# Kernel tuning notes

Measured on AMD Instinct MI355X. Metric: run time of the kernel, lower is better.

The kernel has to match this reference:

```python
import jax, jax.numpy as jnp
import numpy as np

EMB_DIM = 1024
N_HEADS = 16
HEAD_DIM = EMB_DIM // N_HEADS


def setup_inputs() -> dict:
    key = jax.random.key(0)
    ks = jax.random.split(key, 6)
    B, S, D = 2, 2048, EMB_DIM
    scale = 1.0 / np.sqrt(D)
    return {
        "in_data": jax.random.normal(ks[0], (B, S, D), dtype=jnp.float32),
        "Wq": jax.random.normal(ks[1], (D, D), dtype=jnp.float32) * scale,
        "Wk": jax.random.normal(ks[2], (D, D), dtype=jnp.float32) * scale,
        "Wv": jax.random.normal(ks[3], (D, D), dtype=jnp.float32) * scale,
        "Wo": jax.random.normal(ks[4], (D, D), dtype=jnp.float32) * scale,
        "bo": jax.random.normal(ks[5], (D,), dtype=jnp.float32) * 0.01,
    }


def reference(in_data, Wq, Wk, Wv, Wo, bo):
    B, S, D = in_data.shape
    H, Hd = N_HEADS, HEAD_DIM
    # Linear projections (qvbias=False): torch Linear is x @ W.T
    q = in_data @ Wq.T
    k = in_data @ Wk.T
    v = in_data @ Wv.T
    # split heads -> (B, H, S, Hd)
    q = q.reshape(B, S, H, Hd).transpose(0, 2, 1, 3)
    k = k.reshape(B, S, H, Hd).transpose(0, 2, 1, 3)
    v = v.reshape(B, S, H, Hd).transpose(0, 2, 1, 3)
    # scores (B, H, S, S), causal mask applied BEFORE scaling (as in source)
    scores = jnp.einsum("bhqd,bhkd->bhqk", q, k)
    causal = jnp.triu(jnp.ones((S, S), dtype=bool), k=1)
    scores = jnp.where(causal, -jnp.inf, scores)
    scores = scores / jnp.sqrt(jnp.asarray(Hd, dtype=scores.dtype))
    attn = jax.nn.softmax(scores, axis=-1)
    # dropout with drop_rate=0.0 -> identity
    ctx = jnp.einsum("bhqk,bhkd->bhqd", attn, v)
    ctx = ctx.transpose(0, 2, 1, 3).reshape(B, S, D)
    out = ctx @ Wo.T + bo
    return out
```

## Files before the change

kernel.cpp:

```cpp
#include <hip/hip_runtime.h>

typedef _Float16 f16;
typedef _Float16 f16x2 __attribute__((ext_vector_type(2)));
typedef _Float16 f16x4 __attribute__((ext_vector_type(4)));
typedef _Float16 f16x8 __attribute__((ext_vector_type(8)));
typedef float f32x4 __attribute__((ext_vector_type(4)));
typedef int i32x4 __attribute__((ext_vector_type(4)));

#define MFMA(a, b, c) __builtin_amdgcn_mfma_f32_16x16x32_f16((a), (b), (c), 0, 0, 0)

typedef __attribute__((address_space(1))) const void gvoid;
typedef __attribute__((address_space(3))) void lvoid;

__device__ __forceinline__ void gload16(const void* g, void* l) {
    __builtin_amdgcn_global_load_lds((gvoid*)g, (lvoid*)l, 16, 0, 0);
}

__global__ void cast_all(const float* __restrict__ x,
                         const float* __restrict__ w0, const float* __restrict__ w1,
                         const float* __restrict__ w2, const float* __restrict__ w3,
                         f16* __restrict__ xb, f16* __restrict__ wb) {
    const int NX = 4096 * 1024;
    int i = (blockIdx.x * 256 + threadIdx.x) * 4;
    if (i < NX) {
        float4 v = *(const float4*)(x + i);
        f16x4 o = {(f16)v.x, (f16)v.y, (f16)v.z, (f16)v.w};
        *(f16x4*)(xb + i) = o;
    } else {
        int j = i - NX;
        const float* s = (j < (1 << 20)) ? w0 : (j < (2 << 20)) ? w1
                       : (j < (3 << 20)) ? w2 : w3;
        int loc = j & ((1 << 20) - 1);
        float4 v = *(const float4*)(s + loc);
        f16x4 o = {(f16)v.x, (f16)v.y, (f16)v.z, (f16)v.w};
        *(f16x4*)(wb + j) = o;
    }
}

template <bool FINAL>
__global__ void gemm_bt(const f16* __restrict__ A, const f16* __restrict__ Bw,
                        f16* __restrict__ Cf, f16* __restrict__ VTo,
                        float* __restrict__ Co, const float* __restrict__ bias) {
    __shared__ __align__(16) f16 As[128 * 64];
    __shared__ __align__(16) f16 Bs[128 * 64];
    const int tid = threadIdx.x;
    const int lane = tid & 63, wid = tid >> 6;
    const int lo = lane & 15, hi = lane >> 4;
    const int wr = wid >> 1, wc = wid & 1;
    const int m0 = blockIdx.x * 128, n0 = blockIdx.y * 128;
    const char* Ab = (const char*)A;
    const char* Bb = (const char*)(Bw + (size_t)blockIdx.z * (1024 * 1024));

    f32x4 acc[4][4];
#pragma unroll
    for (int i = 0; i < 4; ++i)
#pragma unroll
        for (int j = 0; j < 4; ++j) acc[i][j] = (f32x4){0.f, 0.f, 0.f, 0.f};

    for (int kt = 0; kt < 16; ++kt) {
        const int kb = kt * 128;
#pragma unroll
        for (int rr = 0; rr < 4; ++rr) {
            int o = rr * 4096 + tid * 16;
            int row = o >> 7, colB = o & 127;
            gload16(Ab + (size_t)(m0 + row) * 2048 + kb + colB, (char*)As + o);
            gload16(Bb + (size_t)(n0 + row) * 2048 + kb + colB, (char*)Bs + o);
        }
        __syncthreads();
#pragma unroll
        for (int kc = 0; kc < 2; ++kc) {
            f16x8 af[4], bf[4];
#pragma unroll
            for (int f = 0; f < 4; ++f)
                af[f] = *(const f16x8*)(As + (wr * 64 + f * 16 + lo) * 64 + kc * 32 + hi * 8);
#pragma unroll
            for (int f = 0; f < 4; ++f)
                bf[f] = *(const f16x8*)(Bs + (wc * 64 + f * 16 + lo) * 64 + kc * 32 + hi * 8);
#pragma unroll
            for (int i = 0; i < 4; ++i)
#pragma unroll
                for (int j = 0; j < 4; ++j) acc[i][j] = MFMA(af[i], bf[j], acc[i][j]);
        }
        __syncthreads();
    }

    const int mbase = m0 + wr * 64 + hi * 4;
    const int nbase = n0 + wc * 64 + lo;
    if (FINAL) {
#pragma unroll
        for (int j = 0; j < 4; ++j) {
            float bj = bias[nbase + j * 16];
#pragma unroll
            for (int i = 0; i < 4; ++i)
#pragma unroll
                for (int r = 0; r < 4; ++r)
                    Co[(size_t)(mbase + i * 16 + r) * 1024 + nbase + j * 16] =
                        acc[i][j][r] + bj;
        }
    } else if (blockIdx.z == 2) {
#pragma unroll
        for (int i = 0; i < 4; ++i)
#pragma unroll
            for (int j = 0; j < 4; ++j)
#pragma unroll
                for (int r = 0; r < 4; ++r) {
                    int m = mbase + i * 16 + r, n = nbase + j * 16;
                    VTo[(size_t)((m >> 11) * 1024 + n) * 2048 + (m & 2047)] =
                        (f16)acc[i][j][r];
                }
    } else {
        const float osc = (blockIdx.z == 0) ? 0.18033688f : 1.0f;
        f16* Cz = Cf + (size_t)blockIdx.z * (4096 * 1024);
#pragma unroll
        for (int i = 0; i < 4; ++i)
#pragma unroll
            for (int j = 0; j < 4; ++j)
#pragma unroll
                for (int r = 0; r < 4; ++r)
                    Cz[(size_t)(mbase + i * 16 + r) * 1024 + nbase + j * 16] =
                        (f16)(acc[i][j][r] * osc);
    }
}

__global__ __launch_bounds__(256) void attn(const f16* __restrict__ Q,
                                            const f16* __restrict__ K,
                                            const f16* __restrict__ VT,
                                            f16* __restrict__ CTX) {
    __shared__ __align__(16) f16 K0[64 * 64];
    __shared__ __align__(16) f16 K1[64 * 64];
    __shared__ __align__(16) f16 V0[64 * 64];
    __shared__ __align__(16) f16 V1[64 * 64];
    const int tid = threadIdx.x;
    const int lane = tid & 63, w = tid >> 6;
    const int lo = lane & 15, hi = lane >> 4;
    const int bh = blockIdx.x;
    const int qt = 31 - blockIdx.y;
    const int b = bh >> 4, h = bh & 15;
    const int qw0 = qt * 64 + w * 16;
    const int qglob = qw0 + lo;

    const f16* qrow = Q + (size_t)(b * 2048 + qw0 + lo) * 1024 + h * 64 + hi * 8;
    const f16x8 qa0 = *(const f16x8*)(qrow);
    const f16x8 qa1 = *(const f16x8*)(qrow + 32);

    f32x4 ctx[4];
#pragma unroll
    for (int d = 0; d < 4; ++d) ctx[d] = (f32x4){0.f, 0.f, 0.f, 0.f};
    float mrun = -3e38f, lsum = 0.f;

    const int idx0 = (2 * (hi & 1)) * 16 + lo;
    const int idx1 = idx0 + 16;

    const char* Kb = (const char*)K;
    const char* Vb = (const char*)VT;

    auto stage = [&](f16* Kd, f16* Vd, int t) {
        const int kv0 = t * 64;
#pragma unroll
        for (int rr = 0; rr < 2; ++rr) {
            int o = rr * 4096 + tid * 16;
            int row = o >> 7;
            int colB = (o & 127) ^ ((row & 7) << 4);
            gload16(Kb + (size_t)(b * 2048 + kv0 + row) * 2048 + h * 128 + colB,
                    (char*)Kd + o);
            gload16(Vb + (size_t)(b * 1024 + h * 64 + row) * 4096 + (size_t)kv0 * 2 + colB,
                    (char*)Vd + o);
        }
    };

    auto compute = [&](const f16* Klb, const f16* Vlb, int t) {
        f32x4 s4[4];
        __builtin_amdgcn_s_setprio(1);
#pragma unroll
        for (int fj = 0; fj < 4; ++fj) {
            f32x4 a = (f32x4){0.f, 0.f, 0.f, 0.f};
            const int kv = fj * 16 + lo;
#pragma unroll
            for (int kc = 0; kc < 2; ++kc) {
                const int cb = (kc * 64 + hi * 16) ^ ((kv & 7) << 4);
                f16x8 kf = *(const f16x8*)((const char*)Klb + kv * 128 + cb);
                a = MFMA(kf, kc ? qa1 : qa0, a);
            }
            s4[fj] = a;
        }
        __builtin_amdgcn_s_setprio(0);

        float pv[16];
        if (t == qt) {
#pragma unroll
            for (int fj = 0; fj < 4; ++fj)
#pragma unroll
                for (int r = 0; r < 4; ++r) {
                    const int kvg = t * 64 + fj * 16 + hi * 4 + r;
                    pv[fj * 4 + r] = (kvg > qglob) ? -1e38f : s4[fj][r];
                }
        } else {
#pragma unroll
            for (int fj = 0; fj < 4; ++fj)
#pragma unroll
                for (int r = 0; r < 4; ++r) pv[fj * 4 + r] = s4[fj][r];
        }

        float tm[8];
#pragma unroll
        for (int i = 0; i < 8; ++i) tm[i] = fmaxf(pv[i], pv[i + 8]);
#pragma unroll
        for (int i = 0; i < 4; ++i) tm[i] = fmaxf(tm[i], tm[i + 4]);
        const float mxl = fmaxf(fmaxf(tm[0], tm[1]), fmaxf(tm[2], tm[3]));

        if (__any(mxl > mrun + 8.0f)) {
            float mxg = fmaxf(mxl, __shfl_xor(mxl, 16));
            mxg = fmaxf(mxg, __shfl_xor(mxg, 32));
            const float mnew = fmaxf(mrun, mxg);
            const float corr = __builtin_amdgcn_exp2f(mrun - mnew);
            mrun = mnew;
            lsum *= corr;
#pragma unroll
            for (int d = 0; d < 4; ++d) {
                ctx[d][0] *= corr; ctx[d][1] *= corr;
                ctx[d][2] *= corr; ctx[d][3] *= corr;
            }
        }

#pragma unroll
        for (int i = 0; i < 16; ++i) pv[i] = __builtin_amdgcn_exp2f(pv[i] - mrun);
        float ts[8];
#pragma unroll
        for (int i = 0; i < 8; ++i) ts[i] = pv[i] + pv[i + 8];
#pragma unroll
        for (int i = 0; i < 4; ++i) ts[i] = ts[i] + ts[i + 4];
        lsum += (ts[0] + ts[1]) + (ts[2] + ts[3]);

        int ph[4][2];
#pragma unroll
        for (int fj = 0; fj < 4; ++fj)
#pragma unroll
            for (int r2 = 0; r2 < 2; ++r2) {
                f16x2 hpair = {(f16)pv[fj * 4 + 2 * r2], (f16)pv[fj * 4 + 2 * r2 + 1]};
                ph[fj][r2] = __builtin_bit_cast(int, hpair);
            }

        f16x8 pb[2];
#pragma unroll
        for (int kc = 0; kc < 2; ++kc) {
            i32x4 dw;
#pragma unroll
            for (int j2 = 0; j2 < 4; ++j2) {
                const int idx = (j2 < 2) ? idx0 : idx1;
                int vA = __shfl(ph[2 * kc][j2 & 1], idx);
                int vB = __shfl(ph[2 * kc + 1][j2 & 1], idx);
                dw[j2] = (hi & 2) ? vB : vA;
            }
            pb[kc] = __builtin_bit_cast(f16x8, dw);
        }

        __builtin_amdgcn_s_setprio(1);
#pragma unroll
        for (int df = 0; df < 4; ++df) {
            const int d = df * 16 + lo;
#pragma unroll
            for (int kc = 0; kc < 2; ++kc) {
                const int cb = (kc * 64 + hi * 16) ^ ((d & 7) << 4);
                f16x8 vf = *(const f16x8*)((const char*)Vlb + d * 128 + cb);
                ctx[df] = MFMA(vf, pb[kc], ctx[df]);
            }
        }
        __builtin_amdgcn_s_setprio(0);
    };

    stage(&K0[0], &V0[0], 0);
    for (int t = 0; t <= qt; ++t) {
        __syncthreads();
        if ((t & 1) == 0) {
            if (t < qt) stage(&K1[0], &V1[0], t + 1);
            compute(&K0[0], &V0[0], t);
        } else {
            if (t < qt) stage(&K0[0], &V0[0], t + 1);
            compute(&K1[0], &V1[0], t);
        }
    }

    float lt = lsum + __shfl_xor(lsum, 16);
    lt += __shfl_xor(lt, 32);
    const float inv = 1.0f / lt;
#pragma unroll
    for (int df = 0; df < 4; ++df) {
        f16x4 o = {(f16)(ctx[df][0] * inv), (f16)(ctx[df][1] * inv),
                   (f16)(ctx[df][2] * inv), (f16)(ctx[df][3] * inv)};
        *(f16x4*)(CTX + (size_t)(b * 2048 + qw0 + lo) * 1024 + h * 64 + df * 16 + hi * 4) = o;
    }
}

extern "C" void kernel_launch(void* const* d_in, const int* in_sizes, int n_in,
                              void* d_out, int out_size, void* d_ws, size_t ws_size,
                              hipStream_t stream) {
    const float* x = (const float*)d_in[0];
    const float* wq = (const float*)d_in[1];
    const float* wk = (const float*)d_in[2];
    const float* wv = (const float*)d_in[3];
    const float* wo = (const float*)d_in[4];
    const float* bo = (const float*)d_in[5];

    const size_t M1 = 1024 * 1024;
    f16* VT = (f16*)d_ws;
    f16* Wh = VT + 4 * M1;
    f16* QKV = Wh + 4 * M1;
    f16* Xb = QKV + 8 * M1;
    f16* Q = QKV;
    f16* K = QKV + 4 * M1;
    f16* CTX = QKV + 8 * M1;
    float* out = (float*)d_out;

    cast_all<<<dim3(8192), dim3(256), 0, stream>>>(x, wq, wk, wv, wo, Xb, Wh);
    gemm_bt<false><<<dim3(32, 8, 3), dim3(256), 0, stream>>>(Xb, Wh, QKV, VT, nullptr, nullptr);
    attn<<<dim3(32, 32), dim3(256), 0, stream>>>(Q, K, VT, CTX);
    gemm_bt<true><<<dim3(32, 8, 1), dim3(256), 0, stream>>>(CTX, Wh + 3 * M1, nullptr, nullptr, out, bo);
}
```

Measured before the change: 185.9 us.

## Split-K output projection with atomics and deepen attention KV staging to four buffers

The output projection now splits K four ways across blockIdx.z and accumulates into the output with float atomicAdd. The output is zeroed by extra blocks in the cast kernel, and the bias is added only by the z==0 slice. The aim is more parallelism than the 256-block final GEMM had. Attention now uses four K/V LDS buffers and processes two KV tiles per sync, which halves barriers and prefetches further ahead, at the cost of more LDS and lower occupancy. The atomics add memory traffic and make the summation order nondeterministic.

```diff
diff --git a/kernel.cpp b/kernel.cpp
--- a/kernel.cpp
+++ b/kernel.cpp
@@ -19,9 +19,17 @@
 __global__ void cast_all(const float* __restrict__ x,
                          const float* __restrict__ w0, const float* __restrict__ w1,
                          const float* __restrict__ w2, const float* __restrict__ w3,
-                         f16* __restrict__ xb, f16* __restrict__ wb) {
+                         f16* __restrict__ xb, f16* __restrict__ wb,
+                         float* __restrict__ out0) {
     const int NX = 4096 * 1024;
-    int i = (blockIdx.x * 256 + threadIdx.x) * 4;
+    const int blk = blockIdx.x;
+    if (blk >= 8192) {
+        int idx = (blk - 8192) * 1024 + threadIdx.x * 4;
+        float4 z = {0.f, 0.f, 0.f, 0.f};
+        *(float4*)(out0 + idx) = z;
+        return;
+    }
+    int i = (blk * 256 + threadIdx.x) * 4;
     if (i < NX) {
         float4 v = *(const float4*)(x + i);
         f16x4 o = {(f16)v.x, (f16)v.y, (f16)v.z, (f16)v.w};
@@ -37,10 +45,9 @@
     }
 }
 
-template <bool FINAL>
-__global__ void gemm_bt(const f16* __restrict__ A, const f16* __restrict__ Bw,
-                        f16* __restrict__ Cf, f16* __restrict__ VTo,
-                        float* __restrict__ Co, const float* __restrict__ bias) {
+__global__ void gemm_qkv(const f16* __restrict__ A, const f16* __restrict__ W,
+                         f16* __restrict__ Qo, f16* __restrict__ Ko,
+                         f16* __restrict__ VTo) {
     __shared__ __align__(16) f16 As[128 * 64];
     __shared__ __align__(16) f16 Bs[128 * 64];
     const int tid = threadIdx.x;
@@ -48,8 +55,9 @@
     const int lo = lane & 15, hi = lane >> 4;
     const int wr = wid >> 1, wc = wid & 1;
     const int m0 = blockIdx.x * 128, n0 = blockIdx.y * 128;
+    const int z = blockIdx.z;
     const char* Ab = (const char*)A;
-    const char* Bb = (const char*)(Bw + (size_t)blockIdx.z * (1024 * 1024));
+    const char* Bb = (const char*)(W + (size_t)z * (1024 * 1024));
 
     f32x4 acc[4][4];
 #pragma unroll
@@ -86,39 +94,35 @@
 
     const int mbase = m0 + wr * 64 + hi * 4;
     const int nbase = n0 + wc * 64 + lo;
-    if (FINAL) {
-#pragma unroll
-        for (int j = 0; j < 4; ++j) {
-            float bj = bias[nbase + j * 16];
-#pragma unroll
-            for (int i = 0; i < 4; ++i)
+    if (z == 0) {
+#pragma unroll
+        for (int i = 0; i < 4; ++i)
+#pragma unroll
+            for (int j = 0; j < 4; ++j)
 #pragma unroll
                 for (int r = 0; r < 4; ++r)
-                    Co[(size_t)(mbase + i * 16 + r) * 1024 + nbase + j * 16] =
-                        acc[i][j][r] + bj;
-        }
-    } else if (blockIdx.z == 2) {
+                    Qo[(size_t)(mbase + i * 16 + r) * 1024 + nbase + j * 16] =
+                        (f16)(acc[i][j][r] * 0.18033688f);
+    } else if (z == 1) {
 #pragma unroll
         for (int i = 0; i < 4; ++i)
 #pragma unroll
             for (int j = 0; j < 4; ++j)
 #pragma unroll
+                for (int r = 0; r < 4; ++r)
+                    Ko[(size_t)(mbase + i * 16 + r) * 1024 + nbase + j * 16] =
+                        (f16)acc[i][j][r];
+    } else {
+#pragma unroll
+        for (int i = 0; i < 4; ++i)
+#pragma unroll
+            for (int j = 0; j < 4; ++j)
+#pragma unroll
                 for (int r = 0; r < 4; ++r) {
-                    int m = mbase + i * 16 + r, n = nbase + j * 16;
+                    const int m = mbase + i * 16 + r, n = nbase + j * 16;
                     VTo[(size_t)((m >> 11) * 1024 + n) * 2048 + (m & 2047)] =
                         (f16)acc[i][j][r];
                 }
-    } else {
-        const float osc = (blockIdx.z == 0) ? 0.18033688f : 1.0f;
-        f16* Cz = Cf + (size_t)blockIdx.z * (4096 * 1024);
-#pragma unroll
-        for (int i = 0; i < 4; ++i)
-#pragma unroll
-            for (int j = 0; j < 4; ++j)
-#pragma unroll
-                for (int r = 0; r < 4; ++r)
-                    Cz[(size_t)(mbase + i * 16 + r) * 1024 + nbase + j * 16] =
-                        (f16)(acc[i][j][r] * osc);
     }
 }
 
@@ -128,8 +132,12 @@
                                             f16* __restrict__ CTX) {
     __shared__ __align__(16) f16 K0[64 * 64];
     __shared__ __align__(16) f16 K1[64 * 64];
+    __shared__ __align__(16) f16 K2[64 * 64];
+    __shared__ __align__(16) f16 K3[64 * 64];
     __shared__ __align__(16) f16 V0[64 * 64];
     __shared__ __align__(16) f16 V1[64 * 64];
+    __shared__ __align__(16) f16 V2[64 * 64];
+    __shared__ __align__(16) f16 V3[64 * 64];
     const int tid = threadIdx.x;
     const int lane = tid & 63, w = tid >> 6;
     const int lo = lane & 15, hi = lane >> 4;
@@ -138,6 +146,7 @@
     const int b = bh >> 4, h = bh & 15;
     const int qw0 = qt * 64 + w * 16;
     const int qglob = qw0 + lo;
+    const int nt = qt + 1;
 
     const f16* qrow = Q + (size_t)(b * 2048 + qw0 + lo) * 1024 + h * 64 + hi * 8;
     const f16x8 qa0 = *(const f16x8*)(qrow);
@@ -269,14 +278,19 @@
     };
 
     stage(&K0[0], &V0[0], 0);
-    for (int t = 0; t <= qt; ++t) {
-        __syncthreads();
-        if ((t & 1) == 0) {
-            if (t < qt) stage(&K1[0], &V1[0], t + 1);
-            compute(&K0[0], &V0[0], t);
+    if (nt > 1) stage(&K1[0], &V1[0], 1);
+    for (int p = 0; p < nt; p += 2) {
+        __syncthreads();
+        if (((p >> 1) & 1) == 0) {
+            if (p + 2 < nt) stage(&K2[0], &V2[0], p + 2);
+            if (p + 3 < nt) stage(&K3[0], &V3[0], p + 3);
+            compute(&K0[0], &V0[0], p);
+            if (p + 1 < nt) compute(&K1[0], &V1[0], p + 1);
         } else {
-            if (t < qt) stage(&K0[0], &V0[0], t + 1);
-            compute(&K1[0], &V1[0], t);
+            if (p + 2 < nt) stage(&K0[0], &V0[0], p + 2);
+            if (p + 3 < nt) stage(&K1[0], &V1[0], p + 3);
+            compute(&K2[0], &V2[0], p);
+            if (p + 1 < nt) compute(&K3[0], &V3[0], p + 1);
         }
     }
 
@@ -288,6 +302,66 @@
         f16x4 o = {(f16)(ctx[df][0] * inv), (f16)(ctx[df][1] * inv),
                    (f16)(ctx[df][2] * inv), (f16)(ctx[df][3] * inv)};
         *(f16x4*)(CTX + (size_t)(b * 2048 + qw0 + lo) * 1024 + h * 64 + df * 16 + hi * 4) = o;
+    }
+}
+
+__global__ void gemm_proj(const f16* __restrict__ A, const f16* __restrict__ Bw,
+                          float* __restrict__ Co, const float* __restrict__ bias) {
+    __shared__ __align__(16) f16 As[128 * 64];
+    __shared__ __align__(16) f16 Bs[128 * 64];
+    const int tid = threadIdx.x;
+    const int lane = tid & 63, wid = tid >> 6;
+    const int lo = lane & 15, hi = lane >> 4;
+    const int wr = wid >> 1, wc = wid & 1;
+    const int m0 = blockIdx.x * 128, n0 = blockIdx.y * 128;
+    const int z = blockIdx.z;
+    const char* Ab = (const char*)A;
+    const char* Bb = (const char*)Bw;
+
+    f32x4 acc[4][4];
+#pragma unroll
+    for (int i = 0; i < 4; ++i)
+#pragma unroll
+        for (int j = 0; j < 4; ++j) acc[i][j] = (f32x4){0.f, 0.f, 0.f, 0.f};
+
+    for (int kt = z * 4; kt < z * 4 + 4; ++kt) {
+        const int kb = kt * 128;
+#pragma unroll
+        for (int rr = 0; rr < 4; ++rr) {
+            int o = rr * 4096 + tid * 16;
+            int row = o >> 7, colB = o & 127;
+            gload16(Ab + (size_t)(m0 + row) * 2048 + kb + colB, (char*)As + o);
+            gload16(Bb + (size_t)(n0 + row) * 2048 + kb + colB, (char*)Bs + o);
+        }
+        __syncthreads();
+#pragma unroll
+        for (int kc = 0; kc < 2; ++kc) {
+            f16x8 af[4], bf[4];
+#pragma unroll
+            for (int f = 0; f < 4; ++f)
+                af[f] = *(const f16x8*)(As + (wr * 64 + f * 16 + lo) * 64 + kc * 32 + hi * 8);
+#pragma unroll
+            for (int f = 0; f < 4; ++f)
+                bf[f] = *(const f16x8*)(Bs + (wc * 64 + f * 16 + lo) * 64 + kc * 32 + hi * 8);
+#pragma unroll
+            for (int i = 0; i < 4; ++i)
+#pragma unroll
+                for (int j = 0; j < 4; ++j) acc[i][j] = MFMA(af[i], bf[j], acc[i][j]);
+        }
+        __syncthreads();
+    }
+
+    const int mbase = m0 + wr * 64 + hi * 4;
+    const int nbase = n0 + wc * 64 + lo;
+#pragma unroll
+    for (int j = 0; j < 4; ++j) {
+        const float bj = (z == 0) ? bias[nbase + j * 16] : 0.f;
+#pragma unroll
+        for (int i = 0; i < 4; ++i)
+#pragma unroll
+            for (int r = 0; r < 4; ++r)
+                atomicAdd(&Co[(size_t)(mbase + i * 16 + r) * 1024 + nbase + j * 16],
+                          acc[i][j][r] + bj);
     }
 }
 
@@ -311,8 +385,8 @@
     f16* CTX = QKV + 8 * M1;
     float* out = (float*)d_out;
 
-    cast_all<<<dim3(8192), dim3(256), 0, stream>>>(x, wq, wk, wv, wo, Xb, Wh);
-    gemm_bt<false><<<dim3(32, 8, 3), dim3(256), 0, stream>>>(Xb, Wh, QKV, VT, nullptr, nullptr);
+    cast_all<<<dim3(12288), dim3(256), 0, stream>>>(x, wq, wk, wv, wo, Xb, Wh, out);
+    gemm_qkv<<<dim3(32, 8, 3), dim3(256), 0, stream>>>(Xb, Wh, Q, K, VT);
     attn<<<dim3(32, 32), dim3(256), 0, stream>>>(Q, K, VT, CTX);
-    gemm_bt<true><<<dim3(32, 8, 1), dim3(256), 0, stream>>>(CTX, Wh + 3 * M1, nullptr, nullptr, out, bo);
-}
+    gemm_proj<<<dim3(32, 8, 4), dim3(256), 0, stream>>>(CTX, Wh + 3 * M1, out, bo);
+}
```

Measured after the change: 229.1 us. +23.3%, slower.
